# Kernel optimization log

Hardware: AMD Instinct MI355X
Metric: run time of the kernel (lower is better)

## Reference

```python
import jax, jax.numpy as jnp
import numpy as np

# static config (levels=4, CDA=False branch -> self_attn_4, scale=4, f=False)
SHAPES = [(80, 80), (40, 40), (20, 20), (10, 10)]
D = 256; NH = 8; NL = 4; NP = 4; DFF = 1024; DH = D // NH
L = sum(h * w for h, w in SHAPES)  # 8500
B = 1


def layer_norm(x, g, b, eps=1e-5):
    m = jnp.mean(x, axis=-1, keepdims=True)
    v = jnp.mean((x - m) ** 2, axis=-1, keepdims=True)
    return (x - m) * jax.lax.rsqrt(v + eps) * g + b


def ms_deform_attn_core(value, loc, attn):
    # value: [B, L, NH, DH]; loc: [B, Lq, NH, NL, NP, 2] in [0,1]; attn: [B, Lq, NH, NL, NP]
    Bq, Lq = loc.shape[0], loc.shape[1]
    out = jnp.zeros((Bq, NH, Lq, DH), value.dtype)
    start = 0
    for lvl, (Hl, Wl) in enumerate(SHAPES):
        v = value[:, start:start + Hl * Wl]          # [B, HW, NH, DH]
        start += Hl * Wl
        v = v.transpose(0, 2, 1, 3)                  # [B, NH, HW, DH]
        ll = loc[:, :, :, lvl]                       # [B, Lq, NH, NP, 2]
        # grid_sample semantics: align_corners=False, padding_mode='zeros'
        x = ll[..., 0] * Wl - 0.5
        y = ll[..., 1] * Hl - 0.5
        x0 = jnp.floor(x); y0 = jnp.floor(y)
        acc = jnp.zeros((Bq, NH, Lq, NP, DH), value.dtype)
        for dy in (0, 1):
            for dx in (0, 1):
                xi = x0 + dx; yi = y0 + dy
                w = (1.0 - jnp.abs(x - xi)) * (1.0 - jnp.abs(y - yi))  # [B,Lq,NH,NP]
                valid = (xi >= 0) & (xi < Wl) & (yi >= 0) & (yi < Hl)
                xi_c = jnp.clip(xi, 0, Wl - 1).astype(jnp.int32)
                yi_c = jnp.clip(yi, 0, Hl - 1).astype(jnp.int32)
                lin = (yi_c * Wl + xi_c).transpose(0, 2, 1, 3).reshape(Bq, NH, Lq * NP)
                g = jnp.take_along_axis(v, lin[..., None], axis=2).reshape(Bq, NH, Lq, NP, DH)
                wv = (w * valid.astype(w.dtype)).transpose(0, 2, 1, 3)[..., None]
                acc = acc + g * wv
        aw = attn[:, :, :, lvl].transpose(0, 2, 1, 3)[..., None]  # [B,NH,Lq,NP,1]
        out = out + jnp.sum(acc * aw, axis=3)
    return out.transpose(0, 2, 1, 3).reshape(Bq, Lq, NH * DH)


def setup_inputs():
    key = jax.random.key(0)
    ks = jax.random.split(key, 24)
    s = 0.02
    d = {}
    d['src'] = jax.random.normal(ks[0], (B, L, D), jnp.float32)
    d['pos'] = jax.random.normal(ks[1], (B, L, D), jnp.float32)
    d['reference_points'] = jax.random.uniform(ks[2], (B, L, NL, 2), jnp.float32)
    d['spatial_shapes'] = jnp.array(SHAPES, jnp.int32)
    d['level_start_index'] = jnp.array(np.cumsum([0] + [h * w for h, w in SHAPES[:-1]]), jnp.int32)
    d['scale'] = 4
    # MSDeformAttn params
    d['Wo'] = jax.random.normal(ks[3], (D, NH * NL * NP * 2), jnp.float32) * s
    d['bo'] = jax.random.normal(ks[4], (NH * NL * NP * 2,), jnp.float32) * s
    d['Wa'] = jax.random.normal(ks[5], (D, NH * NL * NP), jnp.float32) * s
    d['ba'] = jax.random.normal(ks[6], (NH * NL * NP,), jnp.float32) * s
    d['Wv'] = jax.random.normal(ks[7], (D, D), jnp.float32) * s
    d['bv'] = jnp.zeros((D,), jnp.float32)
    d['Wout'] = jax.random.normal(ks[8], (D, D), jnp.float32) * s
    d['bout'] = jnp.zeros((D,), jnp.float32)
    # FFN + LayerNorms
    d['W1'] = jax.random.normal(ks[9], (D, DFF), jnp.float32) * s
    d['b1'] = jnp.zeros((DFF,), jnp.float32)
    d['W2'] = jax.random.normal(ks[10], (DFF, D), jnp.float32) * s
    d['b2'] = jnp.zeros((D,), jnp.float32)
    d['g1'] = jnp.ones((D,), jnp.float32); d['be1'] = jnp.zeros((D,), jnp.float32)
    d['g2'] = jnp.ones((D,), jnp.float32); d['be2'] = jnp.zeros((D,), jnp.float32)
    return d


def reference(src, pos, reference_points, spatial_shapes, level_start_index, scale,
              Wo, bo, Wa, ba, Wv, bv, Wout, bout, W1, b1, W2, b2, g1, be1, g2, be2):
    Bq, Lq, _ = src.shape
    q = src + pos  # with_pos_embed
    # sampling offsets & attention weights (softmax over levels*points)
    off = (q @ Wo + bo).reshape(Bq, Lq, NH, NL, NP, 2)
    attn = jax.nn.softmax((q @ Wa + ba).reshape(Bq, Lq, NH, NL * NP), axis=-1)
    attn = attn.reshape(Bq, Lq, NH, NL, NP)
    value = (src @ Wv + bv).reshape(Bq, L, NH, DH)
    # offset normalizer is (W, H) per level
    normalizer = jnp.stack([spatial_shapes[:, 1], spatial_shapes[:, 0]], -1).astype(src.dtype)
    loc = reference_points[:, :, None, :, None, :] + off / normalizer[None, None, None, :, None, :]
    src2 = ms_deform_attn_core(value, loc, attn) @ Wout + bout
    # residual + norm1 (dropout = eval identity)
    x = layer_norm(src + src2, g1, be1)
    # FFN
    ffn = jax.nn.relu(x @ W1 + b1) @ W2 + b2
    x = layer_norm(x + ffn, g2, be2)
    return x
```

## Files before the change

### kernel.cpp

```cpp
#include <hip/hip_runtime.h>
#include <hip/hip_bf16.h>
#include <string.h>

#define D 256
#define NH 8
#define DH 32
#define NL 4
#define NP 4
#define DFF 1024
#define LTOT 8500

typedef __bf16 bf16x8 __attribute__((ext_vector_type(8)));
typedef float floatx4 __attribute__((ext_vector_type(4)));

__device__ inline unsigned bpack(float a, float b) {
    __hip_bfloat16 ha = __float2bfloat16(a), hb = __float2bfloat16(b);
    unsigned short ua, ub;
    memcpy(&ua, &ha, 2); memcpy(&ub, &hb, 2);
    return (unsigned)ua | ((unsigned)ub << 16);
}

__device__ inline void gload16(const void* g, void* l) {
    __builtin_amdgcn_global_load_lds((const __attribute__((address_space(1))) void*)g,
                                     (__attribute__((address_space(3))) void*)l,
                                     16, 0, 0);
}

__global__ void transpose_all(const float* W0, const float* W1_, const float* W2_,
                              const float* W3, const float* W4, const float* W5,
                              __hip_bfloat16* T0, __hip_bfloat16* T1, __hip_bfloat16* T2,
                              __hip_bfloat16* T3, __hip_bfloat16* T4, __hip_bfloat16* T5,
                              const float* src, const float* pos,
                              __hip_bfloat16* qb, __hip_bfloat16* srcb) {
    int id = blockIdx.x;
    if (id >= 736) {
        int idx = (id - 736) * 2048 + threadIdx.x * 8;
        if (idx < LTOT * 256) {
            float4 s0 = *(const float4*)(src + idx);
            float4 s1 = *(const float4*)(src + idx + 4);
            float4 p0 = *(const float4*)(pos + idx);
            float4 p1 = *(const float4*)(pos + idx + 4);
            uint4 us, uq;
            us.x = bpack(s0.x, s0.y); us.y = bpack(s0.z, s0.w);
            us.z = bpack(s1.x, s1.y); us.w = bpack(s1.z, s1.w);
            uq.x = bpack(s0.x + p0.x, s0.y + p0.y); uq.y = bpack(s0.z + p0.z, s0.w + p0.w);
            uq.z = bpack(s1.x + p1.x, s1.y + p1.y); uq.w = bpack(s1.z + p1.z, s1.w + p1.w);
            *(uint4*)(srcb + idx) = us;
            *(uint4*)(qb + idx)  = uq;
        }
        return;
    }
    const int cum[7] = {0, 64, 96, 160, 224, 480, 736};
    int mi = 0;
    while (id >= cum[mi + 1]) mi++;
    int lid = id - cum[mi];
    const float* W; __hip_bfloat16* T; int K, N;
    switch (mi) {
        case 0: W = W0; T = T0; K = 256;  N = 256;  break;
        case 1: W = W1_; T = T1; K = 256; N = 128;  break;
        case 2: W = W2_; T = T2; K = 256; N = 256;  break;
        case 3: W = W3; T = T3; K = 256;  N = 256;  break;
        case 4: W = W4; T = T4; K = 256;  N = 1024; break;
        default: W = W5; T = T5; K = 1024; N = 256; break;
    }
    int ntx = N >> 5;
    int n0 = (lid % ntx) * 32, k0 = (lid / ntx) * 32;
    __shared__ float t[32][33];
    int tx = threadIdx.x & 31, ty = threadIdx.x >> 5;
#pragma unroll
    for (int i = 0; i < 32; i += 8)
        t[ty + i][tx] = W[(size_t)(k0 + ty + i) * N + n0 + tx];
    __syncthreads();
#pragma unroll
    for (int i = 0; i < 32; i += 8)
        T[(size_t)(n0 + ty + i) * K + k0 + tx] = __float2bfloat16(t[tx][ty + i]);
}

__global__ __launch_bounds__(256) void gemm97(
    const __hip_bfloat16* __restrict__ A, const __hip_bfloat16* __restrict__ BT,
    const float* __restrict__ bias, float* __restrict__ Cf, __hip_bfloat16* __restrict__ Cb,
    int M, int N, int K, int relu) {
    constexpr int BM = 128, BN = 128, BK = 32;
    __shared__ __align__(16) __hip_bfloat16 sA[2][BM * BK];
    __shared__ __align__(16) __hip_bfloat16 sB[2][BN * BK];

    int tid = threadIdx.x, wave = tid >> 6, lane = tid & 63;
    int m0 = blockIdx.y * BM, n0 = blockIdx.x * BN;
    int wm = (wave >> 1) * 64, wn = (wave & 1) * 64;

    floatx4 acc[4][4];
#pragma unroll
    for (int i = 0; i < 4; i++)
#pragma unroll
        for (int j = 0; j < 4; j++)
#pragma unroll
            for (int e = 0; e < 4; e++) acc[i][j][e] = 0.f;

    int l4r = lane >> 2;
    int l4c = (lane & 3) * 8;
    int lrow = lane & 15, lk = (lane >> 4) * 8;

    const __hip_bfloat16* aP[2];
    const __hip_bfloat16* bP[2];
#pragma unroll
    for (int i = 0; i < 2; i++) {
        int g = m0 + wave * 32 + i * 16 + l4r;
        if (g >= M) g = M - 1;
        aP[i] = A + (size_t)g * K + l4c;
        bP[i] = BT + (size_t)(n0 + wave * 32 + i * 16 + l4r) * K + l4c;
    }
    int ldsOff = wave * 2048;

#pragma unroll
    for (int i = 0; i < 2; i++) gload16(aP[i], (char*)&sA[0][0] + ldsOff + i * 1024);
#pragma unroll
    for (int i = 0; i < 2; i++) gload16(bP[i], (char*)&sB[0][0] + ldsOff + i * 1024);
    __syncthreads();

    int cur = 0;
    for (int k0 = 0; k0 < K; k0 += BK) {
        int kn = k0 + BK;
        if (kn < K) {
#pragma unroll
            for (int i = 0; i < 2; i++) gload16(aP[i] + kn, (char*)&sA[cur ^ 1][0] + ldsOff + i * 1024);
#pragma unroll
            for (int i = 0; i < 2; i++) gload16(bP[i] + kn, (char*)&sB[cur ^ 1][0] + ldsOff + i * 1024);
        }

        bf16x8 af[4], bfr[4];
#pragma unroll
        for (int tm = 0; tm < 4; tm++)
            af[tm] = *(const bf16x8*)(&sA[cur][(wm + tm * 16 + lrow) * BK + lk]);
#pragma unroll
        for (int tn = 0; tn < 4; tn++)
            bfr[tn] = *(const bf16x8*)(&sB[cur][(wn + tn * 16 + lrow) * BK + lk]);
#pragma unroll
        for (int tm = 0; tm < 4; tm++)
#pragma unroll
            for (int tn = 0; tn < 4; tn++)
                acc[tm][tn] = __builtin_amdgcn_mfma_f32_16x16x32_bf16(af[tm], bfr[tn], acc[tm][tn], 0, 0, 0);
        __syncthreads();
        cur ^= 1;
    }

    int lcol = lane & 15, lr4 = (lane >> 4) * 4;
#pragma unroll
    for (int tm = 0; tm < 4; tm++) {
#pragma unroll
        for (int i = 0; i < 4; i++) {
            int row = m0 + wm + tm * 16 + lr4 + i;
            if (row < M) {
#pragma unroll
                for (int tn = 0; tn < 4; tn++) {
                    int col = n0 + wn + tn * 16 + lcol;
                    float v = acc[tm][tn][i] + bias[col];
                    if (relu) v = fmaxf(v, 0.f);
                    if (Cf) Cf[(size_t)row * N + col] = v;
                    if (Cb) Cb[(size_t)row * N + col] = __float2bfloat16(v);
                }
            }
        }
    }
}

__global__ __launch_bounds__(256) void proj2(
    const __hip_bfloat16* __restrict__ qb, const __hip_bfloat16* __restrict__ srcb,
    const __hip_bfloat16* __restrict__ WoT, const __hip_bfloat16* __restrict__ WaT,
    const __hip_bfloat16* __restrict__ WvT,
    const float* __restrict__ bo, const float* __restrict__ ba, const float* __restrict__ bv,
    float* __restrict__ locb, float* __restrict__ attnb, __hip_bfloat16* __restrict__ valb,
    int M) {
    constexpr int BM = 128, BN = 128, BK = 32, K = 256;
    __shared__ __align__(16) __hip_bfloat16 sA[2][BM * BK];
    __shared__ __align__(16) __hip_bfloat16 sB[2][BN * BK];

    int n0 = blockIdx.x * BN;
    int m0 = blockIdx.y * BM;

    const __hip_bfloat16* BT;
    const __hip_bfloat16* A;
    const float* bias;
    int ncol0, Nout;
    float* Cf; __hip_bfloat16* Cb;
    if (n0 < 256)      { A = qb;   BT = WoT; bias = bo; ncol0 = n0;       Nout = 256; Cf = locb;  Cb = nullptr; }
    else if (n0 < 384) { A = qb;   BT = WaT; bias = ba; ncol0 = 0;        Nout = 128; Cf = attnb; Cb = nullptr; }
    else               { A = srcb; BT = WvT; bias = bv; ncol0 = n0 - 384; Nout = 256; Cf = nullptr; Cb = valb; }

    int tid = threadIdx.x, wave = tid >> 6, lane = tid & 63;
    int wm = (wave >> 1) * 64, wn = (wave & 1) * 64;

    floatx4 acc[4][4];
#pragma unroll
    for (int i = 0; i < 4; i++)
#pragma unroll
        for (int j = 0; j < 4; j++)
#pragma unroll
            for (int e = 0; e < 4; e++) acc[i][j][e] = 0.f;

    int l4r = lane >> 2, l4c = (lane & 3) * 8;
    int lrow = lane & 15, lk = (lane >> 4) * 8;

    const __hip_bfloat16* aP[2];
    const __hip_bfloat16* bP[2];
#pragma unroll
    for (int i = 0; i < 2; i++) {
        int g = m0 + wave * 32 + i * 16 + l4r;
        if (g >= M) g = M - 1;
        aP[i] = A + (size_t)g * K + l4c;
        bP[i] = BT + (size_t)(ncol0 + wave * 32 + i * 16 + l4r) * K + l4c;
    }
    int ldsOff = wave * 2048;

#pragma unroll
    for (int i = 0; i < 2; i++) gload16(aP[i], (char*)&sA[0][0] + ldsOff + i * 1024);
#pragma unroll
    for (int i = 0; i < 2; i++) gload16(bP[i], (char*)&sB[0][0] + ldsOff + i * 1024);
    __syncthreads();

    int cur = 0;
    for (int k0 = 0; k0 < K; k0 += BK) {
        int kn = k0 + BK;
        if (kn < K) {
#pragma unroll
            for (int i = 0; i < 2; i++) gload16(aP[i] + kn, (char*)&sA[cur ^ 1][0] + ldsOff + i * 1024);
#pragma unroll
            for (int i = 0; i < 2; i++) gload16(bP[i] + kn, (char*)&sB[cur ^ 1][0] + ldsOff + i * 1024);
        }

        bf16x8 af[4], bfr[4];
#pragma unroll
        for (int tm = 0; tm < 4; tm++)
            af[tm] = *(const bf16x8*)(&sA[cur][(wm + tm * 16 + lrow) * BK + lk]);
#pragma unroll
        for (int tn = 0; tn < 4; tn++)
            bfr[tn] = *(const bf16x8*)(&sB[cur][(wn + tn * 16 + lrow) * BK + lk]);
#pragma unroll
        for (int tm = 0; tm < 4; tm++)
#pragma unroll
            for (int tn = 0; tn < 4; tn++)
                acc[tm][tn] = __builtin_amdgcn_mfma_f32_16x16x32_bf16(af[tm], bfr[tn], acc[tm][tn], 0, 0, 0);
        __syncthreads();
        cur ^= 1;
    }

    int lcol = lane & 15, lr4 = (lane >> 4) * 4;
#pragma unroll
    for (int tm = 0; tm < 4; tm++) {
#pragma unroll
        for (int i = 0; i < 4; i++) {
            int row = m0 + wm + tm * 16 + lr4 + i;
            if (row < M) {
#pragma unroll
                for (int tn = 0; tn < 4; tn++) {
                    int col = ncol0 + wn + tn * 16 + lcol;
                    float v = acc[tm][tn][i] + bias[col];
                    if (Cf) Cf[(size_t)row * Nout + col] = v;
                    else    Cb[(size_t)row * Nout + col] = __float2bfloat16(v);
                }
            }
        }
    }
}

__global__ __launch_bounds__(256) void deform(const __hip_bfloat16* __restrict__ value,
                                              const float* __restrict__ locraw,
                                              const float* __restrict__ logits,
                                              const float* __restrict__ refp,
                                              __hip_bfloat16* __restrict__ out) {
    __shared__ float wS[4][8][16][4];
    __shared__ int   aS[4][8][16][4];
    int tid = threadIdx.x;
    int q0 = blockIdx.x * 4;

    {
        int sub = tid >> 6, h = (tid >> 3) & 7, t8 = tid & 7;
        int q = q0 + sub;
        const float* lg = logits + q * 128 + h * 16;
        float l0 = lg[t8], l1 = lg[t8 + 8];
        float mx = fmaxf(l0, l1);
#pragma unroll
        for (int m = 1; m < 8; m <<= 1) mx = fmaxf(mx, __shfl_xor(mx, m, 64));
        float e0 = __expf(l0 - mx), e1 = __expf(l1 - mx);
        float s = e0 + e1;
#pragma unroll
        for (int m = 1; m < 8; m <<= 1) s += __shfl_xor(s, m, 64);
        float inv = 1.f / s;

        const int starts[4] = {0, 6400, 8000, 8400};
#pragma unroll
        for (int j = 0; j < 2; j++) {
            int pp = t8 + 8 * j;
            float a = (j ? e1 : e0) * inv;
            int l = pp >> 2;
            int Wl = 80 >> l;
            float nv = (float)Wl;
            float rx = refp[q * 8 + l * 2 + 0];
            float ry = refp[q * 8 + l * 2 + 1];
            float lx = rx + locraw[q * 256 + h * 32 + pp * 2 + 0] / nv;
            float ly = ry + locraw[q * 256 + h * 32 + pp * 2 + 1] / nv;
            float x = lx * nv - 0.5f;
            float y = ly * nv - 0.5f;
            float x0f = floorf(x), y0f = floorf(y);
            float fx = x - x0f, fy = y - y0f;
            int x0 = (int)x0f, y0 = (int)y0f;
            float wts[4] = {(1.f - fx) * (1.f - fy), fx * (1.f - fy),
                            (1.f - fx) * fy,         fx * fy};
            int st = starts[l];
#pragma unroll
            for (int t = 0; t < 4; t++) {
                int xi = x0 + (t & 1), yi = y0 + (t >> 1);
                bool valid = (xi >= 0) & (xi < Wl) & (yi >= 0) & (yi < Wl);
                int xc = min(max(xi, 0), Wl - 1), yc = min(max(yi, 0), Wl - 1);
                wS[sub][h][pp][t] = valid ? wts[t] * a : 0.f;
                aS[sub][h][pp][t] = (st + yc * Wl + xc) * 512 + h * 64;
            }
        }
    }
    __syncthreads();

    int sub = tid >> 6, h = (tid >> 3) & 7, l8 = tid & 7;
    int q = q0 + sub;
    const char* vb = (const char*)value;
    int lo = l8 * 8;
    float a0 = 0.f, a1 = 0.f, a2 = 0.f, a3 = 0.f;
#pragma unroll
    for (int p = 0; p < 16; p++) {
        floatx4 w = *(const floatx4*)&wS[sub][h][p][0];
        int4 av = *(const int4*)&aS[sub][h][p][0];
#pragma unroll
        for (int t = 0; t < 4; t++) {
            int ad = (t == 0) ? av.x : (t == 1) ? av.y : (t == 2) ? av.z : av.w;
            uint2 u = *(const uint2*)(vb + ad + lo);
            float wt = w[t];
            a0 += wt * __uint_as_float(u.x << 16);
            a1 += wt * __uint_as_float(u.x & 0xffff0000u);
            a2 += wt * __uint_as_float(u.y << 16);
            a3 += wt * __uint_as_float(u.y & 0xffff0000u);
        }
    }
    uint2 o;
    o.x = bpack(a0, a1);
    o.y = bpack(a2, a3);
    *(uint2*)((char*)out + q * 512 + h * 64 + l8 * 8) = o;
}

__global__ __launch_bounds__(512) void gemm_ln(
    const __hip_bfloat16* __restrict__ A, const __hip_bfloat16* __restrict__ BT,
    const float* __restrict__ bias, const float* __restrict__ resid,
    const float* __restrict__ g, const float* __restrict__ be,
    float* __restrict__ outf, __hip_bfloat16* __restrict__ outb,
    int M, int K) {
    constexpr int BM = 32, BK = 32;
    __shared__ __align__(16) __hip_bfloat16 sA[2][BM * BK];
    __shared__ __align__(16) __hip_bfloat16 sB[2][256 * BK];
    __shared__ float psum[8][32], psq[8][32], mS[32], rS[32];

    int tid = threadIdx.x;
    int wave = tid >> 6, lane = tid & 63;
    int m0 = blockIdx.x * BM;

    floatx4 acc[2][2];
#pragma unroll
    for (int i = 0; i < 2; i++)
#pragma unroll
        for (int j = 0; j < 2; j++)
#pragma unroll
            for (int e = 0; e < 4; e++) acc[i][j][e] = 0.f;

    int l4r = lane >> 2, l4c = (lane & 3) * 8;
    int lrow = lane & 15, lk = (lane >> 4) * 8;

    int grA = m0 + wave * 16 + l4r;
    if (grA >= M) grA = M - 1;
    const __hip_bfloat16* aP = A + (size_t)grA * K + l4c;
    const __hip_bfloat16* bP[2];
#pragma unroll
    for (int i = 0; i < 2; i++)
        bP[i] = BT + (size_t)(wave * 32 + i * 16 + l4r) * K + l4c;

    if (wave < 2) gload16(aP, (char*)&sA[0][0] + wave * 1024);
#pragma unroll
    for (int i = 0; i < 2; i++) gload16(bP[i], (char*)&sB[0][0] + wave * 2048 + i * 1024);
    __syncthreads();

    int cur = 0;
    for (int k0 = 0; k0 < K; k0 += BK) {
        int kn = k0 + BK;
        if (kn < K) {
            if (wave < 2) gload16(aP + kn, (char*)&sA[cur ^ 1][0] + wave * 1024);
#pragma unroll
            for (int i = 0; i < 2; i++)
                gload16(bP[i] + kn, (char*)&sB[cur ^ 1][0] + wave * 2048 + i * 1024);
        }

        bf16x8 af[2], bfr[2];
#pragma unroll
        for (int tm = 0; tm < 2; tm++)
            af[tm] = *(const bf16x8*)(&sA[cur][(tm * 16 + lrow) * BK + lk]);
#pragma unroll
        for (int tn = 0; tn < 2; tn++)
            bfr[tn] = *(const bf16x8*)(&sB[cur][(wave * 32 + tn * 16 + lrow) * BK + lk]);
#pragma unroll
        for (int tm = 0; tm < 2; tm++)
#pragma unroll
            for (int tn = 0; tn < 2; tn++)
                acc[tm][tn] = __builtin_amdgcn_mfma_f32_16x16x32_bf16(af[tm], bfr[tn], acc[tm][tn], 0, 0, 0);
        __syncthreads();
        cur ^= 1;
    }

    int lcol = lane & 15, quad = lane >> 4;
    float v[2][2][4];
#pragma unroll
    for (int tm = 0; tm < 2; tm++) {
#pragma unroll
        for (int i = 0; i < 4; i++) {
            int row = tm * 16 + quad * 4 + i;
            int grow = m0 + row; if (grow >= M) grow = M - 1;
#pragma unroll
            for (int tn = 0; tn < 2; tn++) {
                int col = wave * 32 + tn * 16 + lcol;
                v[tm][tn][i] = acc[tm][tn][i] + bias[col] + resid[(size_t)grow * 256 + col];
            }
        }
    }

#pragma unroll
    for (int tm = 0; tm < 2; tm++) {
#pragma unroll
        for (int i = 0; i < 4; i++) {
            float s = 0.f, s2 = 0.f;
#pragma unroll
            for (int tn = 0; tn < 2; tn++) { float x = v[tm][tn][i]; s += x; s2 += x * x; }
#pragma unroll
            for (int m = 1; m < 16; m <<= 1) {
                s  += __shfl_xor(s, m, 64);
                s2 += __shfl_xor(s2, m, 64);
            }
            if (lcol == 0) {
                int row = tm * 16 + quad * 4 + i;
                psum[wave][row] = s;
                psq[wave][row]  = s2;
            }
        }
    }
    __syncthreads();
    if (tid < 32) {
        float s = 0.f, s2 = 0.f;
#pragma unroll
        for (int w = 0; w < 8; w++) { s += psum[w][tid]; s2 += psq[w][tid]; }
        float m = s * (1.f / 256.f);
        float var = fmaxf(s2 * (1.f / 256.f) - m * m, 0.f);
        mS[tid] = m;
        rS[tid] = rsqrtf(var + 1e-5f);
    }
    __syncthreads();

#pragma unroll
    for (int tm = 0; tm < 2; tm++) {
#pragma unroll
        for (int i = 0; i < 4; i++) {
            int row = tm * 16 + quad * 4 + i;
            int grow = m0 + row;
            if (grow < M) {
                float m = mS[row], r = rS[row];
#pragma unroll
                for (int tn = 0; tn < 2; tn++) {
                    int col = wave * 32 + tn * 16 + lcol;
                    float o = (v[tm][tn][i] - m) * r * g[col] + be[col];
                    outf[(size_t)grow * 256 + col] = o;
                    if (outb) outb[(size_t)grow * 256 + col] = __float2bfloat16(o);
                }
            }
        }
    }
}

extern "C" void kernel_launch(void* const* d_in, const int* in_sizes, int n_in,
                              void* d_out, int out_size, void* d_ws, size_t ws_size,
                              hipStream_t stream) {
    const float* src  = (const float*)d_in[0];
    const float* pos  = (const float*)d_in[1];
    const float* refp = (const float*)d_in[2];
    const float* Wo   = (const float*)d_in[6];
    const float* bo   = (const float*)d_in[7];
    const float* Wa   = (const float*)d_in[8];
    const float* ba   = (const float*)d_in[9];
    const float* Wv   = (const float*)d_in[10];
    const float* bv   = (const float*)d_in[11];
    const float* Wout = (const float*)d_in[12];
    const float* bout = (const float*)d_in[13];
    const float* W1   = (const float*)d_in[14];
    const float* b1   = (const float*)d_in[15];
    const float* W2   = (const float*)d_in[16];
    const float* b2   = (const float*)d_in[17];
    const float* g1   = (const float*)d_in[18];
    const float* be1  = (const float*)d_in[19];
    const float* g2   = (const float*)d_in[20];
    const float* be2  = (const float*)d_in[21];
    float* out = (float*)d_out;
    char* ws = (char*)d_ws;

    __hip_bfloat16* WoT   = (__hip_bfloat16*)(ws + 0);
    __hip_bfloat16* WaT   = (__hip_bfloat16*)(ws + 131072);
    __hip_bfloat16* WvT   = (__hip_bfloat16*)(ws + 196608);
    __hip_bfloat16* WoutT = (__hip_bfloat16*)(ws + 327680);
    __hip_bfloat16* W1T   = (__hip_bfloat16*)(ws + 458752);
    __hip_bfloat16* W2T   = (__hip_bfloat16*)(ws + 983040);
    float*          locb  = (float*)(ws + 1507328);
    float*          attnb = (float*)(ws + 10211328);
    __hip_bfloat16* valb  = (__hip_bfloat16*)(ws + 14563328);
    __hip_bfloat16* aob   = (__hip_bfloat16*)(ws + 18915328);
    float*          x1    = (float*)(ws + 23267328);
    __hip_bfloat16* x1b   = (__hip_bfloat16*)(ws + 31971328);
    __hip_bfloat16* hb    = (__hip_bfloat16*)(ws + 36323328);
    __hip_bfloat16* qb    = (__hip_bfloat16*)(ws + 36323328);
    __hip_bfloat16* srcb  = (__hip_bfloat16*)(ws + 36323328 + 4352000);

    transpose_all<<<736 + 1063, 256, 0, stream>>>(Wo, Wa, Wv, Wout, W1, W2,
                                                  WoT, WaT, WvT, WoutT, W1T, W2T,
                                                  src, pos, qb, srcb);

    proj2<<<dim3(5, 67), 256, 0, stream>>>(qb, srcb, WoT, WaT, WvT, bo, ba, bv,
                                           locb, attnb, valb, LTOT);

    deform<<<2125, 256, 0, stream>>>(valb, locb, attnb, refp, aob);

    gemm_ln<<<266, 512, 0, stream>>>(aob, WoutT, bout, src, g1, be1, x1, x1b, LTOT, 256);

    gemm97<<<dim3(8, 67), 256, 0, stream>>>(x1b, W1T, b1, nullptr, hb, LTOT, 1024, 256, 1);

    gemm_ln<<<266, 512, 0, stream>>>(hb, W2T, b2, x1, g2, be2, out, nullptr, LTOT, 1024);
}
```

Baseline: 212.5 us.

## Fuse FFN up-projection, ReLU, down-projection and LayerNorm into one kernel

Replaces the separate W1 GEMM (writing the 8500x1024 bf16 hidden tensor to global memory) and the W2 GEMM+LayerNorm kernel with a single kernel. Each 512-thread block handles 32 rows, keeps the ReLU hidden activations in swizzled LDS, then runs the second GEMM and the residual LayerNorm. This removes the global round trip of the hidden tensor and one launch. In exchange, each block re-streams all of W1 and W2 from L2, uses small 32-row tiles with only 266 blocks, and needs about 112KB of LDS, which limits occupancy.

```diff
diff --git a/kernel.cpp b/kernel.cpp
--- a/kernel.cpp
+++ b/kernel.cpp
@@ -76,93 +76,6 @@
         T[(size_t)(n0 + ty + i) * K + k0 + tx] = __float2bfloat16(t[tx][ty + i]);
 }
 
-__global__ __launch_bounds__(256) void gemm97(
-    const __hip_bfloat16* __restrict__ A, const __hip_bfloat16* __restrict__ BT,
-    const float* __restrict__ bias, float* __restrict__ Cf, __hip_bfloat16* __restrict__ Cb,
-    int M, int N, int K, int relu) {
-    constexpr int BM = 128, BN = 128, BK = 32;
-    __shared__ __align__(16) __hip_bfloat16 sA[2][BM * BK];
-    __shared__ __align__(16) __hip_bfloat16 sB[2][BN * BK];
-
-    int tid = threadIdx.x, wave = tid >> 6, lane = tid & 63;
-    int m0 = blockIdx.y * BM, n0 = blockIdx.x * BN;
-    int wm = (wave >> 1) * 64, wn = (wave & 1) * 64;
-
-    floatx4 acc[4][4];
-#pragma unroll
-    for (int i = 0; i < 4; i++)
-#pragma unroll
-        for (int j = 0; j < 4; j++)
-#pragma unroll
-            for (int e = 0; e < 4; e++) acc[i][j][e] = 0.f;
-
-    int l4r = lane >> 2;
-    int l4c = (lane & 3) * 8;
-    int lrow = lane & 15, lk = (lane >> 4) * 8;
-
-    const __hip_bfloat16* aP[2];
-    const __hip_bfloat16* bP[2];
-#pragma unroll
-    for (int i = 0; i < 2; i++) {
-        int g = m0 + wave * 32 + i * 16 + l4r;
-        if (g >= M) g = M - 1;
-        aP[i] = A + (size_t)g * K + l4c;
-        bP[i] = BT + (size_t)(n0 + wave * 32 + i * 16 + l4r) * K + l4c;
-    }
-    int ldsOff = wave * 2048;
-
-#pragma unroll
-    for (int i = 0; i < 2; i++) gload16(aP[i], (char*)&sA[0][0] + ldsOff + i * 1024);
-#pragma unroll
-    for (int i = 0; i < 2; i++) gload16(bP[i], (char*)&sB[0][0] + ldsOff + i * 1024);
-    __syncthreads();
-
-    int cur = 0;
-    for (int k0 = 0; k0 < K; k0 += BK) {
-        int kn = k0 + BK;
-        if (kn < K) {
-#pragma unroll
-            for (int i = 0; i < 2; i++) gload16(aP[i] + kn, (char*)&sA[cur ^ 1][0] + ldsOff + i * 1024);
-#pragma unroll
-            for (int i = 0; i < 2; i++) gload16(bP[i] + kn, (char*)&sB[cur ^ 1][0] + ldsOff + i * 1024);
-        }
-
-        bf16x8 af[4], bfr[4];
-#pragma unroll
-        for (int tm = 0; tm < 4; tm++)
-            af[tm] = *(const bf16x8*)(&sA[cur][(wm + tm * 16 + lrow) * BK + lk]);
-#pragma unroll
-        for (int tn = 0; tn < 4; tn++)
-            bfr[tn] = *(const bf16x8*)(&sB[cur][(wn + tn * 16 + lrow) * BK + lk]);
-#pragma unroll
-        for (int tm = 0; tm < 4; tm++)
-#pragma unroll
-            for (int tn = 0; tn < 4; tn++)
-                acc[tm][tn] = __builtin_amdgcn_mfma_f32_16x16x32_bf16(af[tm], bfr[tn], acc[tm][tn], 0, 0, 0);
-        __syncthreads();
-        cur ^= 1;
-    }
-
-    int lcol = lane & 15, lr4 = (lane >> 4) * 4;
-#pragma unroll
-    for (int tm = 0; tm < 4; tm++) {
-#pragma unroll
-        for (int i = 0; i < 4; i++) {
-            int row = m0 + wm + tm * 16 + lr4 + i;
-            if (row < M) {
-#pragma unroll
-                for (int tn = 0; tn < 4; tn++) {
-                    int col = n0 + wn + tn * 16 + lcol;
-                    float v = acc[tm][tn][i] + bias[col];
-                    if (relu) v = fmaxf(v, 0.f);
-                    if (Cf) Cf[(size_t)row * N + col] = v;
-                    if (Cb) Cb[(size_t)row * N + col] = __float2bfloat16(v);
-                }
-            }
-        }
-    }
-}
-
 __global__ __launch_bounds__(256) void proj2(
     const __hip_bfloat16* __restrict__ qb, const __hip_bfloat16* __restrict__ srcb,
     const __hip_bfloat16* __restrict__ WoT, const __hip_bfloat16* __restrict__ WaT,
@@ -470,6 +383,202 @@
                     float o = (v[tm][tn][i] - m) * r * g[col] + be[col];
                     outf[(size_t)grow * 256 + col] = o;
                     if (outb) outb[(size_t)grow * 256 + col] = __float2bfloat16(o);
+                }
+            }
+        }
+    }
+}
+
+__global__ __launch_bounds__(512) void ffn_fused(
+    const __hip_bfloat16* __restrict__ A,
+    const __hip_bfloat16* __restrict__ W1T,
+    const float* __restrict__ b1,
+    const __hip_bfloat16* __restrict__ W2T,
+    const float* __restrict__ b2,
+    const float* __restrict__ resid,
+    const float* __restrict__ g, const float* __restrict__ be,
+    float* __restrict__ outf, int M) {
+    __shared__ __align__(16) __hip_bfloat16 sA[32 * 256];
+    __shared__ __align__(16) __hip_bfloat16 sH[32 * 1024];
+    __shared__ __align__(16) __hip_bfloat16 sB[2][256 * 32];
+    __shared__ float psum[8][32], psq[8][32], mS[32], rS[32];
+
+    int tid = threadIdx.x, wave = tid >> 6, lane = tid & 63;
+    int m0 = blockIdx.x * 32;
+    int l4r = lane >> 2, l4c = (lane & 3) * 8;
+    int lrow = lane & 15, lk = (lane >> 4) * 8;
+    int swzA = (lrow & 7) << 3;
+
+#pragma unroll
+    for (int i = 0; i < 2; i++) {
+        int ci = (wave * 2 + i) * 64 + lane;
+        int r = ci >> 5, cc = ci & 31;
+        int gr = m0 + r; if (gr >= M) gr = M - 1;
+        int col = (cc * 8) ^ ((r & 7) << 3);
+        gload16(A + (size_t)gr * 256 + col, (char*)sA + ci * 16);
+    }
+
+    for (int c = 0; c < 4; c++) {
+        floatx4 acc[2][2];
+#pragma unroll
+        for (int i = 0; i < 2; i++)
+#pragma unroll
+            for (int j = 0; j < 2; j++)
+#pragma unroll
+                for (int e = 0; e < 4; e++) acc[i][j][e] = 0.f;
+
+        const __hip_bfloat16* bP[2];
+#pragma unroll
+        for (int i = 0; i < 2; i++)
+            bP[i] = W1T + (size_t)(c * 256 + wave * 32 + i * 16 + l4r) * 256 + l4c;
+
+#pragma unroll
+        for (int i = 0; i < 2; i++)
+            gload16(bP[i], (char*)&sB[0][0] + wave * 2048 + i * 1024);
+        __syncthreads();
+
+        int cur = 0;
+        for (int k0 = 0; k0 < 256; k0 += 32) {
+            int kn = k0 + 32;
+            if (kn < 256) {
+#pragma unroll
+                for (int i = 0; i < 2; i++)
+                    gload16(bP[i] + kn, (char*)&sB[cur ^ 1][0] + wave * 2048 + i * 1024);
+            }
+            bf16x8 af[2], bfr[2];
+#pragma unroll
+            for (int tm = 0; tm < 2; tm++)
+                af[tm] = *(const bf16x8*)(&sA[(tm * 16 + lrow) * 256 + ((k0 + lk) ^ swzA)]);
+#pragma unroll
+            for (int tn = 0; tn < 2; tn++)
+                bfr[tn] = *(const bf16x8*)(&sB[cur][(wave * 32 + tn * 16 + lrow) * 32 + lk]);
+#pragma unroll
+            for (int tm = 0; tm < 2; tm++)
+#pragma unroll
+                for (int tn = 0; tn < 2; tn++)
+                    acc[tm][tn] = __builtin_amdgcn_mfma_f32_16x16x32_bf16(af[tm], bfr[tn], acc[tm][tn], 0, 0, 0);
+            __syncthreads();
+            cur ^= 1;
+        }
+
+        int lcol = lane & 15, lr4q = (lane >> 4) * 4;
+#pragma unroll
+        for (int tm = 0; tm < 2; tm++) {
+#pragma unroll
+            for (int ii = 0; ii < 4; ii++) {
+                int row = tm * 16 + lr4q + ii;
+                int swz = (row & 7) << 3;
+#pragma unroll
+                for (int tn = 0; tn < 2; tn++) {
+                    int col = c * 256 + wave * 32 + tn * 16 + lcol;
+                    float v = acc[tm][tn][ii] + b1[col];
+                    v = fmaxf(v, 0.f);
+                    sH[row * 1024 + (col ^ swz)] = __float2bfloat16(v);
+                }
+            }
+        }
+    }
+
+    const __hip_bfloat16* bP2[2];
+#pragma unroll
+    for (int i = 0; i < 2; i++)
+        bP2[i] = W2T + (size_t)(wave * 32 + i * 16 + l4r) * 1024 + l4c;
+#pragma unroll
+    for (int i = 0; i < 2; i++)
+        gload16(bP2[i], (char*)&sB[0][0] + wave * 2048 + i * 1024);
+    __syncthreads();
+
+    floatx4 acc[2][2];
+#pragma unroll
+    for (int i = 0; i < 2; i++)
+#pragma unroll
+        for (int j = 0; j < 2; j++)
+#pragma unroll
+            for (int e = 0; e < 4; e++) acc[i][j][e] = 0.f;
+
+    int cur = 0;
+    for (int k0 = 0; k0 < 1024; k0 += 32) {
+        int kn = k0 + 32;
+        if (kn < 1024) {
+#pragma unroll
+            for (int i = 0; i < 2; i++)
+                gload16(bP2[i] + kn, (char*)&sB[cur ^ 1][0] + wave * 2048 + i * 1024);
+        }
+        bf16x8 af[2], bfr[2];
+#pragma unroll
+        for (int tm = 0; tm < 2; tm++)
+            af[tm] = *(const bf16x8*)(&sH[(tm * 16 + lrow) * 1024 + ((k0 + lk) ^ swzA)]);
+#pragma unroll
+        for (int tn = 0; tn < 2; tn++)
+            bfr[tn] = *(const bf16x8*)(&sB[cur][(wave * 32 + tn * 16 + lrow) * 32 + lk]);
+#pragma unroll
+        for (int tm = 0; tm < 2; tm++)
+#pragma unroll
+            for (int tn = 0; tn < 2; tn++)
+                acc[tm][tn] = __builtin_amdgcn_mfma_f32_16x16x32_bf16(af[tm], bfr[tn], acc[tm][tn], 0, 0, 0);
+        __syncthreads();
+        cur ^= 1;
+    }
+
+    int lcol = lane & 15, quad = lane >> 4;
+    float v[2][2][4];
+#pragma unroll
+    for (int tm = 0; tm < 2; tm++) {
+#pragma unroll
+        for (int i = 0; i < 4; i++) {
+            int row = tm * 16 + quad * 4 + i;
+            int grow = m0 + row; if (grow >= M) grow = M - 1;
+#pragma unroll
+            for (int tn = 0; tn < 2; tn++) {
+                int col = wave * 32 + tn * 16 + lcol;
+                v[tm][tn][i] = acc[tm][tn][i] + b2[col] + resid[(size_t)grow * 256 + col];
+            }
+        }
+    }
+
+#pragma unroll
+    for (int tm = 0; tm < 2; tm++) {
+#pragma unroll
+        for (int i = 0; i < 4; i++) {
+            float s = 0.f, s2 = 0.f;
+#pragma unroll
+            for (int tn = 0; tn < 2; tn++) { float x = v[tm][tn][i]; s += x; s2 += x * x; }
+#pragma unroll
+            for (int m = 1; m < 16; m <<= 1) {
+                s  += __shfl_xor(s, m, 64);
+                s2 += __shfl_xor(s2, m, 64);
+            }
+            if (lcol == 0) {
+                int row = tm * 16 + quad * 4 + i;
+                psum[wave][row] = s;
+                psq[wave][row]  = s2;
+            }
+        }
+    }
+    __syncthreads();
+    if (tid < 32) {
+        float s = 0.f, s2 = 0.f;
+#pragma unroll
+        for (int w = 0; w < 8; w++) { s += psum[w][tid]; s2 += psq[w][tid]; }
+        float m = s * (1.f / 256.f);
+        float var = fmaxf(s2 * (1.f / 256.f) - m * m, 0.f);
+        mS[tid] = m;
+        rS[tid] = rsqrtf(var + 1e-5f);
+    }
+    __syncthreads();
+
+#pragma unroll
+    for (int tm = 0; tm < 2; tm++) {
+#pragma unroll
+        for (int i = 0; i < 4; i++) {
+            int row = tm * 16 + quad * 4 + i;
+            int grow = m0 + row;
+            if (grow < M) {
+                float m = mS[row], r = rS[row];
+#pragma unroll
+                for (int tn = 0; tn < 2; tn++) {
+                    int col = wave * 32 + tn * 16 + lcol;
+                    outf[(size_t)grow * 256 + col] = (v[tm][tn][i] - m) * r * g[col] + be[col];
                 }
             }
         }
@@ -513,9 +622,8 @@
     __hip_bfloat16* aob   = (__hip_bfloat16*)(ws + 18915328);
     float*          x1    = (float*)(ws + 23267328);
     __hip_bfloat16* x1b   = (__hip_bfloat16*)(ws + 31971328);
-    __hip_bfloat16* hb    = (__hip_bfloat16*)(ws + 36323328);
     __hip_bfloat16* qb    = (__hip_bfloat16*)(ws + 36323328);
-    __hip_bfloat16* srcb  = (__hip_bfloat16*)(ws + 36323328 + 4352000);
+    __hip_bfloat16* srcb  = (__hip_bfloat16*)(ws + 40675328);
 
     transpose_all<<<736 + 1063, 256, 0, stream>>>(Wo, Wa, Wv, Wout, W1, W2,
                                                   WoT, WaT, WvT, WoutT, W1T, W2T,
@@ -528,7 +636,5 @@
 
     gemm_ln<<<266, 512, 0, stream>>>(aob, WoutT, bout, src, g1, be1, x1, x1b, LTOT, 256);
 
-    gemm97<<<dim3(8, 67), 256, 0, stream>>>(x1b, W1T, b1, nullptr, hb, LTOT, 1024, 256, 1);
-
-    gemm_ln<<<266, 512, 0, stream>>>(hb, W2T, b2, x1, g2, be2, out, nullptr, LTOT, 1024);
-}
+    ffn_fused<<<266, 512, 0, stream>>>(x1b, W1T, b1, W2T, b2, x1, g2, be2, out, LTOT);
+}
```

Result: slower. 217.8 us (+2.5%).
